# Kernel optimization log

Measured on AMD Instinct MI355X. Metric: run time of the kernel, lower is better.

The kernel has to match this reference:

```python
import jax, jax.numpy as jnp
import numpy as np

D_MODEL, NUM_HEADS, D_HEAD, N_CTX = 768, 12, 64, 2048
BATCH = 2


def setup_inputs() -> dict:
    key = jax.random.key(0)
    kx, kk, kq, kv, ko = jax.random.split(key, 5)
    s = 1.0 / np.sqrt(D_MODEL).astype(np.float32)
    x = jax.random.normal(kx, (BATCH, N_CTX, D_MODEL), dtype=jnp.float32)
    W_K = jax.random.normal(kk, (NUM_HEADS, D_HEAD, D_MODEL), dtype=jnp.float32) * s
    W_Q = jax.random.normal(kq, (NUM_HEADS, D_HEAD, D_MODEL), dtype=jnp.float32) * s
    W_V = jax.random.normal(kv, (NUM_HEADS, D_HEAD, D_MODEL), dtype=jnp.float32) * s
    W_O = jax.random.normal(ko, (D_MODEL, D_HEAD * NUM_HEADS), dtype=jnp.float32) * s
    return {"x": x, "W_K": W_K, "W_Q": W_Q, "W_V": W_V, "W_O": W_O}


def reference(x, W_K, W_Q, W_V, W_O):
    B, P, _ = x.shape
    d_head = W_K.shape[1]
    # per-head projections: [B, H, P, d_head]
    q = jnp.einsum('hed,bpd->bhpe', W_Q, x)
    k = jnp.einsum('hed,bpd->bhpe', W_K, x)
    v = jnp.einsum('hed,bpd->bhpe', W_V, x)
    # causal scores [B, H, Q, K]
    scores = jnp.einsum('bhqe,bhke->bhqk', q, k) / np.sqrt(d_head).astype(np.float32)
    mask = jnp.tril(jnp.ones((P, P), dtype=bool))
    scores = jnp.where(mask, scores, jnp.asarray(-1e9, scores.dtype))
    attn = jax.nn.softmax(scores, axis=-1)
    z = jnp.einsum('bhqk,bhke->bhqe', attn, v)
    # flatten heads head-major: 'b h q e -> b q (h e)'
    z_flat = z.transpose(0, 2, 1, 3).reshape(B, P, -1)
    return jnp.einsum('bpf,df->bpd', z_flat, W_O)
```

## Files before the change

### kernel.cpp

```cpp
#include <hip/hip_runtime.h>
#include <hip/hip_bf16.h>

typedef __attribute__((ext_vector_type(8))) short bf16x8;
typedef __attribute__((ext_vector_type(4))) float f32x4;
typedef __attribute__((ext_vector_type(16))) float f32x16;

static __device__ __forceinline__ unsigned short f2bf(float f) {
  union { float f; unsigned int u; } v; v.f = f;
  unsigned int u = v.u;
  return (unsigned short)((u + 0x7FFFu + ((u >> 16) & 1u)) >> 16);
}

__device__ __forceinline__ void async_ld16(const void* g, void* l) {
  __builtin_amdgcn_global_load_lds(
      (const __attribute__((address_space(1))) unsigned int*)g,
      (__attribute__((address_space(3))) unsigned int*)l, 16, 0, 0);
}

__global__ __launch_bounds__(256) void cvt_all(
    const float* __restrict__ x, const float* __restrict__ wk,
    const float* __restrict__ wq, const float* __restrict__ wv,
    const float* __restrict__ wo,
    unsigned short* __restrict__ x_bf, unsigned short* __restrict__ wkqv4,
    unsigned short* __restrict__ wo4) {
  int i = blockIdx.x * 256 + threadIdx.x;
  int e0 = i * 4;
  if (e0 < 3145728) {
    float4 v = *(const float4*)(x + e0);
    ushort4 r;
    r.x = f2bf(v.x); r.y = f2bf(v.y); r.z = f2bf(v.z); r.w = f2bf(v.w);
    *(ushort4*)(x_bf + e0) = r;
    return;
  }
  int j = e0 - 3145728;
  int a = j / 589824;
  int off = j - a * 589824;
  int nl = off / 768;
  int k = off - nl * 768;
  const float* src;
  unsigned short* dst;
  int m;
  float scale = 1.0f;
  if (a == 0)      { src = wk; m = nl;        dst = wkqv4; }
  else if (a == 1) { src = wq; m = 768 + nl;  dst = wkqv4; scale = 0.18033688011112042f; }
  else if (a == 2) { src = wv; m = 1536 + nl; dst = wkqv4; }
  else             { src = wo; m = nl;        dst = wo4; }
  float4 v = *(const float4*)(src + off);
  long idx = ((long)(m >> 4) * 24 + (k >> 5)) * 512 + (m & 15) * 32 + (k & 31);
  ushort4 r;
  r.x = f2bf(v.x * scale); r.y = f2bf(v.y * scale);
  r.z = f2bf(v.z * scale); r.w = f2bf(v.w * scale);
  *(ushort4*)(dst + idx) = r;
}

template <int MODE>
__device__ __forceinline__ void gemm_body(
    const unsigned short* __restrict__ A,
    const unsigned short* __restrict__ B4,
    void* __restrict__ outK, void* __restrict__ outQ, void* __restrict__ outV,
    int m0, int n0,
    unsigned short (*As)[8192]) {
  const int tid = threadIdx.x;
  const int w = tid >> 6;
  const int l = tid & 63;
  const int g = l >> 4;
  const int c = l & 15;
  const int wr = w >> 1, wc = w & 1;

  f32x4 acc[4][3];
#pragma unroll
  for (int i = 0; i < 4; i++)
#pragma unroll
    for (int j = 0; j < 3; j++) acc[i][j] = (f32x4){0.f, 0.f, 0.f, 0.f};

  const int lrow = l >> 3;
  const int lcolx = ((l & 7) ^ lrow) * 8;
  const unsigned short* pB = B4 + (long)((n0 >> 4) + wc * 3) * 12288 + c * 32 + g * 8;

  auto stageA = [&](int buf, int kt) {
    const int k0 = kt * 64;
#pragma unroll
    for (int cc = 0; cc < 4; ++cc) {
      int chunk = cc * 4 + w;
      int row = chunk * 8 + lrow;
      async_ld16(A + (long)(m0 + row) * 768 + k0 + lcolx, &As[buf][chunk * 512]);
    }
  };
  auto loadB = [&](bf16x8 (*b)[3], int kt) {
#pragma unroll
    for (int ks = 0; ks < 2; ++ks)
#pragma unroll
      for (int ni = 0; ni < 3; ++ni)
        b[ks][ni] = *(const bf16x8*)(pB + (long)ni * 12288 + (kt * 2 + ks) * 512);
  };

  bf16x8 b0[2][3], b1[2][3];
  stageA(0, 0);
  loadB(b0, 0);

#pragma unroll
  for (int kt = 0; kt < 12; kt += 2) {
    if (kt + 1 < 12) loadB(b1, kt + 1);
    __builtin_amdgcn_sched_barrier(0);
    asm volatile("s_waitcnt vmcnt(6)" ::: "memory");
    __builtin_amdgcn_sched_barrier(0);
    __builtin_amdgcn_s_barrier();
    __builtin_amdgcn_sched_barrier(0);
    if (kt + 1 < 12) stageA(1, kt + 1);
#pragma unroll
    for (int ks = 0; ks < 2; ++ks) {
      bf16x8 a[4];
#pragma unroll
      for (int mi = 0; mi < 4; ++mi) {
        int row = wr * 64 + mi * 16 + c;
        int col = (ks * 32 + g * 8) ^ ((row & 7) * 8);
        a[mi] = *(const bf16x8*)&As[0][row * 64 + col];
      }
#pragma unroll
      for (int mi = 0; mi < 4; ++mi)
#pragma unroll
        for (int ni = 0; ni < 3; ++ni)
          acc[mi][ni] = __builtin_amdgcn_mfma_f32_16x16x32_bf16(a[mi], b0[ks][ni], acc[mi][ni], 0, 0, 0);
    }
    if (kt + 2 < 12) loadB(b0, kt + 2);
    __builtin_amdgcn_sched_barrier(0);
    if (kt + 2 < 12) {
      asm volatile("s_waitcnt vmcnt(6)" ::: "memory");
    } else {
      asm volatile("s_waitcnt vmcnt(0)" ::: "memory");
    }
    __builtin_amdgcn_sched_barrier(0);
    __builtin_amdgcn_s_barrier();
    __builtin_amdgcn_sched_barrier(0);
    if (kt + 2 < 12) stageA(0, kt + 2);
#pragma unroll
    for (int ks = 0; ks < 2; ++ks) {
      bf16x8 a[4];
#pragma unroll
      for (int mi = 0; mi < 4; ++mi) {
        int row = wr * 64 + mi * 16 + c;
        int col = (ks * 32 + g * 8) ^ ((row & 7) * 8);
        a[mi] = *(const bf16x8*)&As[1][row * 64 + col];
      }
#pragma unroll
      for (int mi = 0; mi < 4; ++mi)
#pragma unroll
        for (int ni = 0; ni < 3; ++ni)
          acc[mi][ni] = __builtin_amdgcn_mfma_f32_16x16x32_bf16(a[mi], b1[ks][ni], acc[mi][ni], 0, 0, 0);
    }
  }

  if (MODE == 1) {
    float* O = (float*)outK;
#pragma unroll
    for (int mi = 0; mi < 4; ++mi)
#pragma unroll
      for (int ni = 0; ni < 3; ++ni)
#pragma unroll
        for (int r = 0; r < 4; ++r) {
          int m = m0 + wr * 64 + mi * 16 + g * 4 + r;
          int n = n0 + wc * 48 + ni * 16 + c;
          O[(long)m * 768 + n] = acc[mi][ni][r];
        }
  } else {
    const int which = (n0 >= 1536) ? 2 : (n0 >= 768 ? 1 : 0);
    const int nb = n0 - which * 768;
    const int b = m0 >> 11;
    if (which == 2) {
#pragma unroll
      for (int mi = 0; mi < 4; ++mi)
#pragma unroll
        for (int ni = 0; ni < 3; ++ni) {
          int e = nb + wc * 48 + ni * 16 + c;
          int h = e >> 6, el = e & 63;
          long bh = b * 12 + h;
          int p0 = (m0 & 2047) + wr * 64 + mi * 16 + g * 4;
          long idx = bh * 131072 + (p0 >> 4) * 1024 + el * 16 + (p0 & 15);
          ushort4 pk;
          pk.x = f2bf(acc[mi][ni][0]); pk.y = f2bf(acc[mi][ni][1]);
          pk.z = f2bf(acc[mi][ni][2]); pk.w = f2bf(acc[mi][ni][3]);
          *(ushort4*)&((unsigned short*)outV)[idx] = pk;
        }
    } else {
#pragma unroll
      for (int mi = 0; mi < 4; ++mi)
#pragma unroll
        for (int ni = 0; ni < 3; ++ni)
#pragma unroll
          for (int r = 0; r < 4; ++r) {
            int m = m0 + wr * 64 + mi * 16 + g * 4 + r;
            int nn = nb + wc * 48 + ni * 16 + c;
            int p = m & 2047;
            int h = nn >> 6, e = nn & 63;
            unsigned short val = f2bf(acc[mi][ni][r]);
            long bh = b * 12 + h;
            if (which == 0) {
              long idx = bh * 131072 + (p >> 5) * 2048 + (e >> 4) * 512 + (p & 31) * 16 + (e & 15);
              ((unsigned short*)outK)[idx] = val;
            } else {
              ((unsigned short*)outQ)[((bh * 2048 + p) << 6) + e] = val;
            }
          }
    }
  }
}

__global__ __launch_bounds__(256) void gemm_qkv(
    const unsigned short* __restrict__ A,
    const unsigned short* __restrict__ Wkqv4,
    unsigned short* __restrict__ k4b, unsigned short* __restrict__ qb,
    unsigned short* __restrict__ v4b) {
  __shared__ __align__(16) unsigned short As[2][8192];
  const int lb = blockIdx.x;
  const int xcd = lb & 7, idx = lb >> 3;
  const int mg = xcd >> 1, ng = xcd & 1;
  const int mi = idx / 12, ni = idx - 12 * mi;
  gemm_body<0>(A, Wkqv4, k4b, qb, v4b, (mg * 8 + mi) * 128, (ng * 12 + ni) * 96, As);
}

__global__ __launch_bounds__(256) void gemm_out(
    const unsigned short* __restrict__ A,
    const unsigned short* __restrict__ Wo4,
    float* __restrict__ out) {
  __shared__ __align__(16) unsigned short As[2][8192];
  const int lb = blockIdx.x;
  const int xcd = lb & 7, idx = lb >> 3;
  const int mi = idx >> 3, ni = idx & 7;
  gemm_body<1>(A, Wo4, out, nullptr, nullptr, (xcd * 4 + mi) * 128, ni * 96, As);
}

__global__ __launch_bounds__(256) void attn(
    const unsigned short* __restrict__ Q,
    const unsigned short* __restrict__ K4,
    const unsigned short* __restrict__ V4,
    unsigned short* __restrict__ Z) {
  __shared__ float2 Opart[3][16][64];
  __shared__ float Lpart[3][32];
  __shared__ float Linv[32];
  const int bx = blockIdx.x;
  const int xcd = bx & 7;
  const int idx = bx >> 3;
  const int bh = xcd * 3 + (idx >> 6);
  const int c = 63 - (idx & 63);
  const int tid = threadIdx.x;
  const int w = tid >> 6;
  const int l = tid & 63;
  const int ql = l & 31;
  const int hi = l >> 5;
  const int b = bh / 12, hd = bh - b * 12;
  const long base = (long)bh * 2048 * 64;
  const int q0 = c * 32;

  bf16x8 qf[4];
  {
    const unsigned short* qp = Q + base + (long)(q0 + ql) * 64 + hi * 8;
#pragma unroll
    for (int d = 0; d < 4; ++d) qf[d] = *(const bf16x8*)(qp + d * 16);
  }

  f32x16 o0, o1;
#pragma unroll
  for (int r = 0; r < 16; ++r) { o0[r] = 0.f; o1[r] = 0.f; }
  float lsum = 0.f;

  const unsigned short* kp = K4 + (long)bh * 131072 + ql * 16 + hi * 8;
  const unsigned short* vp = V4 + (long)bh * 131072 + ql * 16 + hi * 8;

  auto loadsub = [&](bf16x8* kf, bf16x8* v0, bf16x8* v1, int s) {
    const unsigned short* kps = kp + (long)s * 2048;
#pragma unroll
    for (int d = 0; d < 4; ++d) kf[d] = *(const bf16x8*)(kps + d * 512);
    const unsigned short* vps = vp + (long)s * 2048;
    v0[0] = *(const bf16x8*)(vps);
    v0[1] = *(const bf16x8*)(vps + 1024);
    v1[0] = *(const bf16x8*)(vps + 512);
    v1[1] = *(const bf16x8*)(vps + 1536);
  };

  auto compute = [&](const bf16x8* kf, const bf16x8* v0, const bf16x8* v1, bool diag) {
    __builtin_amdgcn_s_setprio(1);
    f32x16 s_;
#pragma unroll
    for (int r = 0; r < 16; ++r) s_[r] = 0.f;
#pragma unroll
    for (int d = 0; d < 4; ++d)
      s_ = __builtin_amdgcn_mfma_f32_32x32x16_bf16(kf[d], qf[d], s_, 0, 0, 0);
    __builtin_amdgcn_s_setprio(0);
    if (diag) {
#pragma unroll
      for (int r = 0; r < 16; ++r) {
        int krow = (r & 3) + 8 * (r >> 2) + 4 * hi;
        s_[r] = (krow <= ql) ? s_[r] : -1e30f;
      }
    }
    float p[16];
#pragma unroll
    for (int r = 0; r < 16; ++r) { p[r] = exp2f(s_[r]); lsum += p[r]; }
    unsigned int wpk[8];
#pragma unroll
    for (int i = 0; i < 8; ++i)
      asm("v_cvt_pk_bf16_f32 %0, %1, %2" : "=v"(wpk[i]) : "v"(p[2 * i]), "v"(p[2 * i + 1]));
    asm volatile("v_permlane32_swap_b32 %0, %1" : "+v"(wpk[0]), "+v"(wpk[2]));
    asm volatile("v_permlane32_swap_b32 %0, %1" : "+v"(wpk[1]), "+v"(wpk[3]));
    asm volatile("v_permlane32_swap_b32 %0, %1" : "+v"(wpk[4]), "+v"(wpk[6]));
    asm volatile("v_permlane32_swap_b32 %0, %1" : "+v"(wpk[5]), "+v"(wpk[7]));
    union { unsigned int u[4]; bf16x8 v; } f0, f1;
    f0.u[0] = wpk[0]; f0.u[1] = wpk[1]; f0.u[2] = wpk[2]; f0.u[3] = wpk[3];
    f1.u[0] = wpk[4]; f1.u[1] = wpk[5]; f1.u[2] = wpk[6]; f1.u[3] = wpk[7];
    __builtin_amdgcn_s_setprio(1);
    o0 = __builtin_amdgcn_mfma_f32_32x32x16_bf16(f0.v, v0[0], o0, 0, 0, 0);
    o1 = __builtin_amdgcn_mfma_f32_32x32x16_bf16(f0.v, v1[0], o1, 0, 0, 0);
    o0 = __builtin_amdgcn_mfma_f32_32x32x16_bf16(f1.v, v0[1], o0, 0, 0, 0);
    o1 = __builtin_amdgcn_mfma_f32_32x32x16_bf16(f1.v, v1[1], o1, 0, 0, 0);
    __builtin_amdgcn_s_setprio(0);
  };

  int s = w;
  if (s <= c) {
    bf16x8 kfA[4], vA0[2], vA1[2], kfB[4], vB0[2], vB1[2];
    loadsub(kfA, vA0, vA1, s);
    while (s + 8 <= c) {
      loadsub(kfB, vB0, vB1, s + 4);
      compute(kfA, vA0, vA1, false);
      loadsub(kfA, vA0, vA1, s + 8);
      compute(kfB, vB0, vB1, false);
      s += 8;
    }
    if (s + 4 <= c) {
      loadsub(kfB, vB0, vB1, s + 4);
      compute(kfA, vA0, vA1, false);
      compute(kfB, vB0, vB1, (s + 4) == c);
    } else {
      compute(kfA, vA0, vA1, s == c);
    }
  }

  lsum += __shfl_xor(lsum, 32);

  if (w) {
#pragma unroll
    for (int r = 0; r < 16; ++r) Opart[w - 1][r][l] = make_float2(o0[r], o1[r]);
    if (l < 32) Lpart[w - 1][l] = lsum;
  }
  __syncthreads();
  if (w == 0) {
    float ltot = lsum + Lpart[0][ql] + Lpart[1][ql] + Lpart[2][ql];
    if (l < 32) Linv[l] = 1.0f / ltot;
#pragma unroll
    for (int r = 0; r < 16; ++r) {
      float2 t0 = Opart[0][r][l], t1 = Opart[1][r][l], t2 = Opart[2][r][l];
      o0[r] += t0.x + t1.x + t2.x;
      o1[r] += t0.y + t1.y + t2.y;
    }
#pragma unroll
    for (int r = 0; r < 16; ++r) {
      int qr = (r & 3) + 8 * (r >> 2) + 4 * hi;
      float li = Linv[qr];
      unsigned short* zp = Z + ((long)(b * 2048 + q0 + qr) * 768 + hd * 64 + ql);
      zp[0]  = f2bf(o0[r] * li);
      zp[32] = f2bf(o1[r] * li);
    }
  }
}

extern "C" void kernel_launch(void* const* d_in, const int* in_sizes, int n_in,
                              void* d_out, int out_size, void* d_ws, size_t ws_size,
                              hipStream_t stream) {
  const float* x  = (const float*)d_in[0];
  const float* wk = (const float*)d_in[1];
  const float* wq = (const float*)d_in[2];
  const float* wv = (const float*)d_in[3];
  const float* wo = (const float*)d_in[4];

  unsigned short* ws = (unsigned short*)d_ws;
  unsigned short* x_bf  = ws;
  unsigned short* wkqv4 = x_bf + 3145728;
  unsigned short* wo4   = wkqv4 + 1769472;
  unsigned short* qb    = wo4 + 589824;
  unsigned short* k4b   = qb + 3145728;
  unsigned short* v4b   = k4b + 3145728;
  unsigned short* zb    = v4b + 3145728;

  cvt_all<<<5376, 256, 0, stream>>>(x, wk, wq, wv, wo, x_bf, wkqv4, wo4);
  gemm_qkv<<<768, 256, 0, stream>>>(x_bf, wkqv4, k4b, qb, v4b);
  attn<<<1536, 256, 0, stream>>>(qb, k4b, v4b, zb);
  gemm_out<<<256, 256, 0, stream>>>(zb, wo4, (float*)d_out);
}
```

Before: 81.46 us.

## Share K/V tiles in LDS across two query chunks per attention block

Each attention block now handles two adjacent 32-row query chunks, with two waves per chunk splitting the key range. K/V tiles of 64 keys are staged into double-buffered LDS with async global-to-LDS loads and then read by all four waves. Before, every wave loaded its own K/V from global memory. The change halves the grid and cuts redundant global K/V traffic. In exchange it adds a block-wide barrier on every step, and waves idle on the diagonal step when one chunk has fewer keys than the other.

```diff
diff --git a/kernel.cpp b/kernel.cpp
--- a/kernel.cpp
+++ b/kernel.cpp
@@ -234,22 +234,29 @@
     const unsigned short* __restrict__ K4,
     const unsigned short* __restrict__ V4,
     unsigned short* __restrict__ Z) {
-  __shared__ float2 Opart[3][16][64];
-  __shared__ float Lpart[3][32];
-  __shared__ float Linv[32];
+  __shared__ __align__(16) unsigned short Ks[2][4096];
+  __shared__ __align__(16) unsigned short Vs[2][4096];
+  __shared__ float2 Opart[2][16][64];
+  __shared__ float Lpart[2][32];
   const int bx = blockIdx.x;
   const int xcd = bx & 7;
   const int idx = bx >> 3;
-  const int bh = xcd * 3 + (idx >> 6);
-  const int c = 63 - (idx & 63);
+  const int q3 = idx / 3;
+  const int hh = idx - q3 * 3;
+  const int bh = xcd * 3 + hh;
+  const int pp = 31 - q3;
   const int tid = threadIdx.x;
   const int w = tid >> 6;
+  const int cw = w & 1;
+  const int pr = w >> 1;
   const int l = tid & 63;
   const int ql = l & 31;
   const int hi = l >> 5;
+  const int cq = 2 * pp + cw;
   const int b = bh / 12, hd = bh - b * 12;
   const long base = (long)bh * 2048 * 64;
-  const int q0 = c * 32;
+  const long base4 = (long)bh * 131072;
+  const int q0 = cq * 32;
 
   bf16x8 qf[4];
   {
@@ -263,21 +270,26 @@
   for (int r = 0; r < 16; ++r) { o0[r] = 0.f; o1[r] = 0.f; }
   float lsum = 0.f;
 
-  const unsigned short* kp = K4 + (long)bh * 131072 + ql * 16 + hi * 8;
-  const unsigned short* vp = V4 + (long)bh * 131072 + ql * 16 + hi * 8;
-
-  auto loadsub = [&](bf16x8* kf, bf16x8* v0, bf16x8* v1, int s) {
-    const unsigned short* kps = kp + (long)s * 2048;
-#pragma unroll
-    for (int d = 0; d < 4; ++d) kf[d] = *(const bf16x8*)(kps + d * 512);
-    const unsigned short* vps = vp + (long)s * 2048;
-    v0[0] = *(const bf16x8*)(vps);
-    v0[1] = *(const bf16x8*)(vps + 1024);
-    v1[0] = *(const bf16x8*)(vps + 512);
-    v1[1] = *(const bf16x8*)(vps + 1536);
+  auto stage = [&](int buf, int t) {
+#pragma unroll
+    for (int i = 0; i < 2; ++i) {
+      int ch = w * 2 + i;
+      async_ld16(K4 + base4 + (long)t * 4096 + ch * 512 + l * 8, &Ks[buf][ch * 512]);
+      async_ld16(V4 + base4 + (long)t * 4096 + ch * 512 + l * 8, &Vs[buf][ch * 512]);
+    }
   };
 
-  auto compute = [&](const bf16x8* kf, const bf16x8* v0, const bf16x8* v1, bool diag) {
+  auto compute = [&](int cur, int sl, bool diag) {
+    const unsigned short* ksrc = &Ks[cur][sl * 2048 + ql * 16 + hi * 8];
+    bf16x8 kf[4];
+#pragma unroll
+    for (int d = 0; d < 4; ++d) kf[d] = *(const bf16x8*)(ksrc + d * 512);
+    const unsigned short* vsrc = &Vs[cur][sl * 2048 + ql * 16 + hi * 8];
+    bf16x8 v00 = *(const bf16x8*)(vsrc);
+    bf16x8 v01 = *(const bf16x8*)(vsrc + 1024);
+    bf16x8 v10 = *(const bf16x8*)(vsrc + 512);
+    bf16x8 v11 = *(const bf16x8*)(vsrc + 1536);
+
     __builtin_amdgcn_s_setprio(1);
     f32x16 s_;
 #pragma unroll
@@ -308,54 +320,44 @@
     f0.u[0] = wpk[0]; f0.u[1] = wpk[1]; f0.u[2] = wpk[2]; f0.u[3] = wpk[3];
     f1.u[0] = wpk[4]; f1.u[1] = wpk[5]; f1.u[2] = wpk[6]; f1.u[3] = wpk[7];
     __builtin_amdgcn_s_setprio(1);
-    o0 = __builtin_amdgcn_mfma_f32_32x32x16_bf16(f0.v, v0[0], o0, 0, 0, 0);
-    o1 = __builtin_amdgcn_mfma_f32_32x32x16_bf16(f0.v, v1[0], o1, 0, 0, 0);
-    o0 = __builtin_amdgcn_mfma_f32_32x32x16_bf16(f1.v, v0[1], o0, 0, 0, 0);
-    o1 = __builtin_amdgcn_mfma_f32_32x32x16_bf16(f1.v, v1[1], o1, 0, 0, 0);
+    o0 = __builtin_amdgcn_mfma_f32_32x32x16_bf16(f0.v, v00, o0, 0, 0, 0);
+    o1 = __builtin_amdgcn_mfma_f32_32x32x16_bf16(f0.v, v10, o1, 0, 0, 0);
+    o0 = __builtin_amdgcn_mfma_f32_32x32x16_bf16(f1.v, v01, o0, 0, 0, 0);
+    o1 = __builtin_amdgcn_mfma_f32_32x32x16_bf16(f1.v, v11, o1, 0, 0, 0);
     __builtin_amdgcn_s_setprio(0);
   };
 
-  int s = w;
-  if (s <= c) {
-    bf16x8 kfA[4], vA0[2], vA1[2], kfB[4], vB0[2], vB1[2];
-    loadsub(kfA, vA0, vA1, s);
-    while (s + 8 <= c) {
-      loadsub(kfB, vB0, vB1, s + 4);
-      compute(kfA, vA0, vA1, false);
-      loadsub(kfA, vA0, vA1, s + 8);
-      compute(kfB, vB0, vB1, false);
-      s += 8;
-    }
-    if (s + 4 <= c) {
-      loadsub(kfB, vB0, vB1, s + 4);
-      compute(kfA, vA0, vA1, false);
-      compute(kfB, vB0, vB1, (s + 4) == c);
-    } else {
-      compute(kfA, vA0, vA1, s == c);
-    }
+  stage(0, 0);
+  for (int t = 0; t <= pp; ++t) {
+    const int cur = t & 1;
+    asm volatile("s_waitcnt vmcnt(0)" ::: "memory");
+    __builtin_amdgcn_sched_barrier(0);
+    __builtin_amdgcn_s_barrier();
+    __builtin_amdgcn_sched_barrier(0);
+    if (t < pp) stage(cur ^ 1, t + 1);
+    const int s = 2 * t + pr;
+    if (s <= cq) compute(cur, pr, s == cq);
   }
 
   lsum += __shfl_xor(lsum, 32);
-
-  if (w) {
-#pragma unroll
-    for (int r = 0; r < 16; ++r) Opart[w - 1][r][l] = make_float2(o0[r], o1[r]);
-    if (l < 32) Lpart[w - 1][l] = lsum;
+  if (pr == 1) {
+#pragma unroll
+    for (int r = 0; r < 16; ++r) Opart[cw][r][l] = make_float2(o0[r], o1[r]);
+    if (l < 32) Lpart[cw][l] = lsum;
   }
   __syncthreads();
-  if (w == 0) {
-    float ltot = lsum + Lpart[0][ql] + Lpart[1][ql] + Lpart[2][ql];
-    if (l < 32) Linv[l] = 1.0f / ltot;
+  if (pr == 0) {
+    float linv = 1.0f / (lsum + Lpart[cw][ql]);
 #pragma unroll
     for (int r = 0; r < 16; ++r) {
-      float2 t0 = Opart[0][r][l], t1 = Opart[1][r][l], t2 = Opart[2][r][l];
-      o0[r] += t0.x + t1.x + t2.x;
-      o1[r] += t0.y + t1.y + t2.y;
+      float2 t2 = Opart[cw][r][l];
+      o0[r] += t2.x;
+      o1[r] += t2.y;
     }
 #pragma unroll
     for (int r = 0; r < 16; ++r) {
       int qr = (r & 3) + 8 * (r >> 2) + 4 * hi;
-      float li = Linv[qr];
+      float li = __shfl(linv, qr);
       unsigned short* zp = Z + ((long)(b * 2048 + q0 + qr) * 768 + hd * 64 + ql);
       zp[0]  = f2bf(o0[r] * li);
       zp[32] = f2bf(o1[r] * li);
@@ -383,6 +385,6 @@
 
   cvt_all<<<5376, 256, 0, stream>>>(x, wk, wq, wv, wo, x_bf, wkqv4, wo4);
   gemm_qkv<<<768, 256, 0, stream>>>(x_bf, wkqv4, k4b, qb, v4b);
-  attn<<<1536, 256, 0, stream>>>(qb, k4b, v4b, zb);
+  attn<<<768, 256, 0, stream>>>(qb, k4b, v4b, zb);
   gemm_out<<<256, 256, 0, stream>>>(zb, wo4, (float*)d_out);
 }
```

New measurement: 90.25 us. +10.8%, slower.
